# Kernel tuning notes

Measured on AMD Instinct MI355X. Metric: run time of the kernel, lower is better.

Reference implementation:

```python
import jax, jax.numpy as jnp
import numpy as np

TAU_MEM = 10.0
TAU_SYN = (5.0,)
THRESHOLD = 1.0
DT = 1.0
TAU_RHO = 1.0
SCALE_RHO = 1.0


def _psp_kernel(tau_mem, tau_syn, dt):
    # double-exponential EPSP kernel over a 10*tau_mem window (sinabs convention)
    t = np.arange(0.0, 10.0 * tau_mem, dt)
    return tau_syn / (tau_syn - tau_mem) * (np.exp(-t / tau_syn) - np.exp(-t / tau_mem))


def setup_inputs() -> dict:
    key = jax.random.key(0)
    n_syn, B, N, T = 1, 32, 1024, 1024
    # sparse binary spike raster, layout (n_syn, batch, neurons, time)
    binary_input = (jax.random.uniform(key, (n_syn, B, N, T)) < 0.05).astype(jnp.float32)
    epsp_kernel = jnp.asarray(
        np.stack([_psp_kernel(TAU_MEM, ts, DT) for ts in TAU_SYN]), dtype=jnp.float32
    )  # (n_syn, K)
    t = np.arange(0.0, 10.0 * TAU_MEM, DT)
    ref_kernel = jnp.asarray(np.exp(-t / TAU_MEM) * THRESHOLD, dtype=jnp.float32)  # (K,)
    return {"binary_input": binary_input, "epsp_kernel": epsp_kernel, "ref_kernel": ref_kernel}


def _generate_epsp(x, kernel):
    # x: (n_syn, B, N, T); kernel: (n_syn, K). Causal conv along time per synapse.
    n_syn, B, N, T = x.shape
    K = kernel.shape[1]
    xr = jnp.transpose(x.reshape(n_syn, B * N, T), (1, 0, 2))  # (B*N, n_syn, T)
    w = kernel[:, None, ::-1]  # (n_syn, 1, K), flipped -> true convolution
    y = jax.lax.conv_general_dilated(
        xr, w, window_strides=(1,), padding=[(K - 1, 0)], feature_group_count=n_syn
    )  # causal: y[t] = sum_k x[t-k] * kernel[k]
    return jnp.transpose(y, (1, 0, 2)).reshape(n_syn, B, N, T)


def _spike_function(vmem, ref_kernel, threshold, tau_rho, scale_rho):
    # Refractory kernel is threshold*exp(-t/tau_mem): its effect is an exponential
    # state r that decays by alpha each step and jumps by n_spikes*threshold.
    alpha = ref_kernel[1] / ref_kernel[0]
    a = tau_rho * threshold

    def sur(v):
        # antiderivative of SLAYER surrogate pdf (scale/a)*exp(-|v-th|/a);
        # only its gradient matters (straight-through trick below)
        u = v - threshold
        return scale_rho * jnp.sign(u) * (1.0 - jnp.exp(-jnp.abs(u) / a))

    def step(r, v_t):
        v = v_t - r  # membrane after accumulated refractory response
        n_hard = jnp.maximum(jnp.floor(v / threshold), 0.0)  # multi-spike per bin
        n = jax.lax.stop_gradient(n_hard - sur(v)) + sur(v)
        r_next = (r + n * threshold) * alpha
        return r_next, n

    vT = jnp.moveaxis(vmem, -1, 0)  # (T, B, N)
    r0 = jnp.zeros(vmem.shape[:-1], vmem.dtype)
    _, spikes = jax.lax.scan(step, r0, vT)
    return jnp.moveaxis(spikes, 0, -1)  # (B, N, T)


def reference(binary_input, epsp_kernel, ref_kernel):
    vsyn = _generate_epsp(binary_input, epsp_kernel)  # (n_syn, B, N, T)
    vmem = vsyn.sum(0)  # (B, N, T)
    return _spike_function(vmem, ref_kernel, THRESHOLD, TAU_RHO, SCALE_RHO)
```

## Files before the change

kernel.cpp:

```cpp
#include <hip/hip_runtime.h>
#include <cmath>


#define T_LEN   1024
#define NT      32
#define RING    4
#define VROWW   33
#define VSLOTD  (64 * VROWW)
#define LDS_FLG (RING * VSLOTD * 8)
#define LDS_TOT (LDS_FLG + 33 * 4)

__global__ __launch_bounds__(256, 2)
void spiking_fwd(const float* __restrict__ x, const float* __restrict__ rk,
                 float* __restrict__ out,
                 double a_m, double a_s, double am100, double as100)
{
    __shared__ __align__(16) unsigned char lds[LDS_TOT];
    int* const flags = (int*)(lds + LDS_FLG);
    int* const consp = flags + NT;

    const int tid = threadIdx.x, wid = tid >> 6, lane = tid & 63;
    const int n0 = blockIdx.x * 64;
    const unsigned vsw = (lane >> 4) & 3;

    if (tid <= NT) flags[tid] = 0;
    __syncthreads();

    if (wid < 3) {
        int pwarm = 0, ptot = 0, pt0 = 0, gt0 = 0;
        if (wid == 0) { pt0 = 0;   ptot = 17; pwarm = 0; gt0 = 0;  }
        if (wid == 1) { pt0 = 256; ptot = 17; pwarm = 9; gt0 = 8;  }
        if (wid == 2) { pt0 = 512; ptot = 16; pwarm = 9; gt0 = 16; }
        const float* xrow = x + (size_t)(n0 + lane) * T_LEN + pt0;

        double s_m = 0.0, s_s = 0.0;
        unsigned b0 = 0, b1 = 0, b2 = 0, b3 = 0;
        float cur[32], nxt[32];
        #pragma unroll
        for (int j = 0; j < 8; ++j) {
            float4 t = *(const float4*)(xrow + j * 4);
            cur[4*j+0]=t.x; cur[4*j+1]=t.y; cur[4*j+2]=t.z; cur[4*j+3]=t.w;
        }

        for (int li = 0; li < ptot; ++li) {
            if (li + 1 < ptot) {
                #pragma unroll
                for (int j = 0; j < 8; ++j) {
                    float4 t = *(const float4*)(xrow + (li+1)*32 + j*4);
                    nxt[4*j+0]=t.x; nxt[4*j+1]=t.y; nxt[4*j+2]=t.z; nxt[4*j+3]=t.w;
                }
            }
            const unsigned wmask = (b0 >> 28) | (b1 << 4);
            unsigned bcur = 0;
            const int gt = gt0 + li;
            if (li >= pwarm) {
                while (gt - __hip_atomic_load(consp, __ATOMIC_ACQUIRE,
                                              __HIP_MEMORY_SCOPE_WORKGROUP) >= RING)
                    __builtin_amdgcn_s_sleep(1);
                double* vrow = (double*)lds
                             + (size_t)(gt & (RING-1)) * VSLOTD + (size_t)lane * VROWW;
                #pragma unroll
                for (int k = 0; k < 32; ++k) {
                    const float  xf = cur[k];
                    const double xc = (double)xf;
                    const unsigned bd = (wmask >> k) & 1u;
                    s_m = fma(a_m, s_m, xc - (bd ? am100 : 0.0));
                    s_s = fma(a_s, s_s, xc - (bd ? as100 : 0.0));
                    vrow[k ^ vsw] = s_m - s_s;
                    if (xf != 0.0f) bcur |= (1u << k);
                }
                __hip_atomic_store(&flags[gt], 1, __ATOMIC_RELEASE,
                                   __HIP_MEMORY_SCOPE_WORKGROUP);
            } else {
                #pragma unroll
                for (int k = 0; k < 32; ++k) {
                    const float  xf = cur[k];
                    const double xc = (double)xf;
                    const unsigned bd = (wmask >> k) & 1u;
                    s_m = fma(a_m, s_m, xc - (bd ? am100 : 0.0));
                    s_s = fma(a_s, s_s, xc - (bd ? as100 : 0.0));
                    if (xf != 0.0f) bcur |= (1u << k);
                }
            }
            b0 = b1; b1 = b2; b2 = b3; b3 = bcur;
            #pragma unroll
            for (int i2 = 0; i2 < 32; ++i2) cur[i2] = nxt[i2];
        }
    } else {
        const double alpha = (double)rk[1] / (double)rk[0];
        double r = 0.0;
        float* const gdst0 = out + (size_t)(n0 + lane) * T_LEN;

#define STEP1(VMV, OO) do {                                   \
            double v_ = (VMV) - r;                            \
            double n_ = fmax(floor(v_), 0.0);                 \
            r = (r + n_) * alpha;                             \
            OO = (float)n_;                                   \
        } while (0)

#define PREF(VM, H) do {                                      \
            _Pragma("unroll")                                 \
            for (int k2 = 0; k2 < 8; ++k2)                    \
                (VM)[k2] = vrow[((H)*8 + k2) ^ vsw];          \
        } while (0)

#define SCANCH(VM, H) do {                                    \
            float4 o0, o1;                                    \
            STEP1((VM)[0], o0.x); STEP1((VM)[1], o0.y);       \
            STEP1((VM)[2], o0.z); STEP1((VM)[3], o0.w);       \
            STEP1((VM)[4], o1.x); STEP1((VM)[5], o1.y);       \
            STEP1((VM)[6], o1.z); STEP1((VM)[7], o1.w);       \
            *(float4*)(gdst + (H)*8)     = o0;                \
            *(float4*)(gdst + (H)*8 + 4) = o1;                \
        } while (0)

        for (int gt = 0; gt < NT; ++gt) {
            while (!__hip_atomic_load(&flags[gt], __ATOMIC_ACQUIRE,
                                      __HIP_MEMORY_SCOPE_WORKGROUP))
                __builtin_amdgcn_s_sleep(1);
            const double* vrow = (const double*)lds
                               + (size_t)(gt & (RING-1)) * VSLOTD
                               + (size_t)lane * VROWW;
            float* gdst = gdst0 + gt * 32;

            double vA[8], vB[8];
            PREF(vA, 0);
            PREF(vB, 1);
            SCANCH(vA, 0);
            PREF(vA, 2);
            SCANCH(vB, 1);
            PREF(vB, 3);
            SCANCH(vA, 2);
            SCANCH(vB, 3);

            __hip_atomic_store(consp, gt + 1, __ATOMIC_RELEASE,
                               __HIP_MEMORY_SCOPE_WORKGROUP);
        }
#undef SCANCH
#undef PREF
#undef STEP1
    }
}

extern "C" void kernel_launch(void* const* d_in, const int* in_sizes, int n_in,
                              void* d_out, int out_size, void* d_ws, size_t ws_size,
                              hipStream_t stream)
{
    const float* x  = (const float*)d_in[0];
    const float* rk = (const float*)d_in[2];
    float* out = (float*)d_out;

    const int neurons = in_sizes[0] / T_LEN;

    const double a_m   = std::exp(-0.1);
    const double a_s   = std::exp(-0.2);
    const double am100 = std::exp(-10.0);
    const double as100 = std::exp(-20.0);

    dim3 grid(neurons / 64), block(256);
    hipLaunchKernelGGL(spiking_fwd, grid, block, 0, stream,
                       x, rk, out, a_m, a_s, am100, as100);
}
```

Before: 72.27 us.

## Coalesce producer input loads through an LDS staging tile and shrink ring

Measured after the change: 141.2 us. 95.4% more time.

```diff
diff --git a/kernel.cpp b/kernel.cpp
--- a/kernel.cpp
+++ b/kernel.cpp
@@ -4,10 +4,13 @@
 
 #define T_LEN   1024
 #define NT      32
-#define RING    4
+#define RING    2
 #define VROWW   33
 #define VSLOTD  (64 * VROWW)
-#define LDS_FLG (RING * VSLOTD * 8)
+#define SROWW   36
+#define STAGEW  (64 * SROWW)
+#define LDS_STG (RING * VSLOTD * 8)
+#define LDS_FLG (LDS_STG + 3 * STAGEW * 4)
 #define LDS_TOT (LDS_FLG + 33 * 4)
 
 __global__ __launch_bounds__(256, 2)
@@ -31,28 +34,40 @@
         if (wid == 0) { pt0 = 0;   ptot = 17; pwarm = 0; gt0 = 0;  }
         if (wid == 1) { pt0 = 256; ptot = 17; pwarm = 9; gt0 = 8;  }
         if (wid == 2) { pt0 = 512; ptot = 16; pwarm = 9; gt0 = 16; }
-        const float* xrow = x + (size_t)(n0 + lane) * T_LEN + pt0;
+        const float* xbase = x + (size_t)n0 * T_LEN + pt0;
+        const int rowq = lane >> 3, colq = lane & 7;
+        float* const stg = (float*)(lds + LDS_STG) + wid * STAGEW;
+
+        float4 g[8];
+        #pragma unroll
+        for (int j = 0; j < 8; ++j)
+            g[j] = *(const float4*)(xbase + (size_t)(rowq + 8*j) * T_LEN + colq * 4);
+        #pragma unroll
+        for (int j = 0; j < 8; ++j)
+            *(float4*)(stg + (rowq + 8*j) * SROWW + colq * 4) = g[j];
 
         double s_m = 0.0, s_s = 0.0;
         unsigned b0 = 0, b1 = 0, b2 = 0, b3 = 0;
-        float cur[32], nxt[32];
-        #pragma unroll
-        for (int j = 0; j < 8; ++j) {
-            float4 t = *(const float4*)(xrow + j * 4);
-            cur[4*j+0]=t.x; cur[4*j+1]=t.y; cur[4*j+2]=t.z; cur[4*j+3]=t.w;
-        }
 
         for (int li = 0; li < ptot; ++li) {
+            float4 xc4[8];
+            const float* srow = stg + lane * SROWW;
+            #pragma unroll
+            for (int gq = 0; gq < 8; ++gq)
+                xc4[gq] = *(const float4*)(srow + gq * 4);
+
             if (li + 1 < ptot) {
                 #pragma unroll
-                for (int j = 0; j < 8; ++j) {
-                    float4 t = *(const float4*)(xrow + (li+1)*32 + j*4);
-                    nxt[4*j+0]=t.x; nxt[4*j+1]=t.y; nxt[4*j+2]=t.z; nxt[4*j+3]=t.w;
-                }
+                for (int j = 0; j < 8; ++j)
+                    g[j] = *(const float4*)(xbase + (size_t)(rowq + 8*j) * T_LEN
+                                            + (li + 1) * 32 + colq * 4);
             }
+
             const unsigned wmask = (b0 >> 28) | (b1 << 4);
             unsigned bcur = 0;
             const int gt = gt0 + li;
+            const float* xcf = (const float*)xc4;
+
             if (li >= pwarm) {
                 while (gt - __hip_atomic_load(consp, __ATOMIC_ACQUIRE,
                                               __HIP_MEMORY_SCOPE_WORKGROUP) >= RING)
@@ -61,7 +76,7 @@
                              + (size_t)(gt & (RING-1)) * VSLOTD + (size_t)lane * VROWW;
                 #pragma unroll
                 for (int k = 0; k < 32; ++k) {
-                    const float  xf = cur[k];
+                    const float  xf = xcf[k];
                     const double xc = (double)xf;
                     const unsigned bd = (wmask >> k) & 1u;
                     s_m = fma(a_m, s_m, xc - (bd ? am100 : 0.0));
@@ -74,7 +89,7 @@
             } else {
                 #pragma unroll
                 for (int k = 0; k < 32; ++k) {
-                    const float  xf = cur[k];
+                    const float  xf = xcf[k];
                     const double xc = (double)xf;
                     const unsigned bd = (wmask >> k) & 1u;
                     s_m = fma(a_m, s_m, xc - (bd ? am100 : 0.0));
@@ -83,8 +98,12 @@
                 }
             }
             b0 = b1; b1 = b2; b2 = b3; b3 = bcur;
-            #pragma unroll
-            for (int i2 = 0; i2 < 32; ++i2) cur[i2] = nxt[i2];
+
+            if (li + 1 < ptot) {
+                #pragma unroll
+                for (int j = 0; j < 8; ++j)
+                    *(float4*)(stg + (rowq + 8*j) * SROWW + colq * 4) = g[j];
+            }
         }
     } else {
         const double alpha = (double)rk[1] / (double)rk[0];
```
